# Performance work log

Hardware: AMD Instinct MI355X
Metric: run time of the kernel (lower is better)

Reference implementation:

```python
import jax, jax.numpy as jnp
import numpy as np

B, S, D, NH = 2, 1024, 2048, 8
QK, V, I = 1024, 2048, 8192  # qk_dim = D/2, v_dim = D, intermediate = 4D
CAP = 15.0
EPS = 1e-6


def setup_inputs() -> dict:
    key = jax.random.key(0)
    ks = jax.random.split(key, 12)
    sc = D ** -0.5
    return {
        "x": jax.random.normal(ks[0], (B, S, D), jnp.float32),
        "Wq": jax.random.normal(ks[1], (D, QK), jnp.float32) * sc,
        "Wk": jax.random.normal(ks[2], (D, QK), jnp.float32) * sc,
        "Wv": jax.random.normal(ks[3], (D, V), jnp.float32) * sc,
        "Wo": jax.random.normal(ks[4], (D, V), jnp.float32) * sc,
        "Wi": jax.random.normal(ks[5], (D, NH), jnp.float32) * sc,
        "bi": -10.0 * jnp.ones((NH,), jnp.float32),   # xLSTM input-gate bias init
        "Wf": jax.random.normal(ks[6], (D, NH), jnp.float32) * sc,
        "bf": jnp.linspace(3.0, 6.0, NH, dtype=jnp.float32),  # forget-gate bias init
        "mh_norm_w": jnp.ones((V,), jnp.float32),
        "Wout": jax.random.normal(ks[7], (V, D), jnp.float32) * (V ** -0.5),
        "rms1_w": jnp.ones((D,), jnp.float32),
        "Wgate": jax.random.normal(ks[8], (D, I), jnp.float32) * sc,
        "Wup": jax.random.normal(ks[9], (D, I), jnp.float32) * sc,
        "Wdown": jax.random.normal(ks[10], (I, D), jnp.float32) * (I ** -0.5),
        "rms2_w": jnp.ones((D,), jnp.float32),
    }


def soft_cap(x, cap=CAP):
    return cap * jnp.tanh(x / cap)


def rms_norm(x, w, eps=EPS):
    xf = x.astype(jnp.float32)
    var = jnp.mean(xf * xf, axis=-1, keepdims=True)
    return (w * (xf * jax.lax.rsqrt(var + eps))).astype(x.dtype)


def mlstm_stabilized(q, k, v, i, f):
    # q,k: [B,NH,S,DQK]; v: [B,NH,S,DV]; i,f: [B,NH,S] (soft-capped preacts)
    dqk = q.shape[-1]
    logf = jax.nn.log_sigmoid(f.astype(jnp.float32))
    lfc = jnp.cumsum(logf, axis=-1)                         # [B,NH,S]
    tri = jnp.tril(jnp.ones((S, S), bool))
    # log decay D[t,s] = sum_{j=s+1..t} log sig(f_j) + i_s  (causal)
    logD = jnp.where(tri, lfc[..., :, None] - lfc[..., None, :], -jnp.inf) + i[..., None, :]
    m = jnp.max(logD, axis=-1, keepdims=True)               # [B,NH,S,1] stabilizer
    Dm = jnp.exp(logD - m)
    scores = jnp.einsum("bhsd,bhtd->bhst", q, k) * (dqk ** -0.5) * Dm
    n = jnp.maximum(jnp.abs(scores.sum(-1, keepdims=True)), jnp.exp(-m))
    return jnp.einsum("bhst,bhtv->bhsv", scores, v) / (n + EPS)  # [B,NH,S,DV]


def xlstm_layer(x, Wq, Wk, Wv, Wo, Wi, bi, Wf, bf, mh_norm_w, Wout):
    q = (x @ Wq).reshape(B, S, NH, -1).transpose(0, 2, 1, 3)
    k = (x @ Wk).reshape(B, S, NH, -1).transpose(0, 2, 1, 3)
    v = (x @ Wv).reshape(B, S, NH, -1).transpose(0, 2, 1, 3)
    o_preact = x @ Wo                                       # [B,S,V]
    i = soft_cap(x @ Wi + bi).transpose(0, 2, 1)            # [B,NH,S]
    f = soft_cap(x @ Wf + bf).transpose(0, 2, 1)
    h = mlstm_stabilized(q, k, v, i, f)                     # [B,NH,S,DV]
    h = h.transpose(0, 2, 1, 3)                             # [B,S,NH,DV]
    # multi-head RMS norm over per-head value dim
    hf = h.astype(jnp.float32)
    var = jnp.mean(hf * hf, axis=-1, keepdims=True)
    hn = (hf * jax.lax.rsqrt(var + EPS)).reshape(B, S, V) * mh_norm_w
    h_out = jax.nn.sigmoid(o_preact) * hn                   # output gate
    return h_out @ Wout


def reference(x, Wq, Wk, Wv, Wo, Wi, bi, Wf, bf, mh_norm_w, Wout, rms1_w,
              Wgate, Wup, Wdown, rms2_w):
    residual = x
    h = xlstm_layer(x, Wq, Wk, Wv, Wo, Wi, bi, Wf, bf, mh_norm_w, Wout)
    h = residual + rms_norm(h, rms1_w)
    mlp = (jax.nn.silu(h @ Wgate) * (h @ Wup)) @ Wdown
    return h + rms_norm(mlp, rms2_w)
```

## Files before the change

kernel.cpp:

```cpp
#include <hip/hip_runtime.h>
#include <hip/hip_bf16.h>

#define TOKENS 2048
#define DMODEL 2048
#define SEQ    1024
#define QKVO   6144

typedef __attribute__((ext_vector_type(8))) short bf16x8;
typedef __attribute__((ext_vector_type(4))) short bf16x4;
typedef __attribute__((ext_vector_type(4))) float f32x4;
typedef __attribute__((ext_vector_type(8))) unsigned short u16x8;
typedef __attribute__((ext_vector_type(4))) unsigned short u16x4;

__device__ __forceinline__ float sigmoidf_(float x) { return 1.f / (1.f + expf(-x)); }
__device__ __forceinline__ float softcapf_(float x) { return 15.f * tanhf(x * (1.f / 15.f)); }
__device__ __forceinline__ float logsigf_(float x) {
  return (x >= 0.f) ? -log1pf(expf(-x)) : (x - log1pf(expf(x)));
}
__device__ __forceinline__ unsigned short f2bf(float f) {
  unsigned u = __builtin_bit_cast(unsigned, f);
  u += 0x7FFFu + ((u >> 16) & 1u);
  return (unsigned short)(u >> 16);
}
__device__ __forceinline__ float bf2f(unsigned short b) {
  unsigned u = ((unsigned)b) << 16;
  return __builtin_bit_cast(float, u);
}

typedef __attribute__((address_space(3))) void lds_void;
typedef const __attribute__((address_space(1))) void gmem_void;
__device__ __forceinline__ void gload16(const void* g, void* l) {
  __builtin_amdgcn_global_load_lds((gmem_void*)g, (lds_void*)l, 16, 0, 0);
}
__device__ __forceinline__ unsigned lds_off(const void* p) {
  return (unsigned)(size_t)(__attribute__((address_space(3))) const void*)p;
}

#if defined(__has_builtin)
#if __has_builtin(__builtin_amdgcn_mfma_f32_16x16x16bf16_1k)
#define HAVE_MFMA16 1
#endif
#endif

__device__ __forceinline__ f32x4 mfma16_bf16(bf16x4 a, bf16x4 b, f32x4 c) {
#ifdef HAVE_MFMA16
  return __builtin_amdgcn_mfma_f32_16x16x16bf16_1k(a, b, c, 0, 0, 0);
#else
  f32x4 d;
  asm volatile("v_mfma_f32_16x16x16_bf16 %0, %1, %2, %3"
               : "=v"(d) : "v"(a), "v"(b), "v"(c));
  return d;
#endif
}

__device__ __forceinline__ bf16x4 tr_read(unsigned addr) {
  bf16x4 d;
  asm volatile("ds_read_b64_tr_b16 %0, %1" : "=v"(d) : "v"(addr));
  return d;
}

__device__ __forceinline__ void remap_block(int& bm, int& bn) {
  const int nbx = gridDim.x, nby = gridDim.y;
  const int bid = blockIdx.y * nbx + blockIdx.x;
  const int q = (nbx * nby) >> 3;
  const int lid = (bid & 7) * q + (bid >> 3);
  bm = lid % nby;
  bn = lid / nby;
}

template <int EPI>
__global__ __launch_bounds__(512) void gemm256(
    const unsigned short* __restrict__ A, const unsigned short* __restrict__ BT,
    void* __restrict__ Cout, int M, int N, int K, int ldk) {
  __shared__ unsigned short lds[3][2][8192];
  const int tid = threadIdx.x;
  int bm, bn;
  remap_block(bm, bn);
  const int m0 = bm * 256, n0 = bn * 256;
  const int wid = tid >> 6, lane = tid & 63;
  const int wr = wid >> 2, wc = wid & 3;
  const int fr = lane & 15, fq = lane >> 4;
  const size_t kz = (size_t)blockIdx.z * K;

  const f32x4 zero = {0.f, 0.f, 0.f, 0.f};
  f32x4 acc[8][4];
#pragma unroll
  for (int m = 0; m < 8; ++m)
#pragma unroll
    for (int n = 0; n < 4; ++n) acc[m][n] = zero;

  const int sr = tid >> 2;
  const int sc = tid & 3;
  const int sgc = sc ^ ((sr + (sr >> 2)) & 3);
  const unsigned short* Asrc = A + kz + (size_t)(m0 + sr) * ldk + sgc * 8;
  const unsigned short* Bsrc = BT + kz + (size_t)(n0 + sr) * ldk + sgc * 8;
  const size_t hstep = (size_t)128 * ldk;
  const int ldst = sr * 32 + sc * 8;

  const int rsw = (fq ^ ((fr + (fr >> 2)) & 3)) * 8;
  const int arow0 = wr * 128 + fr;
  const int brow0 = wc * 64 + fr;

  auto stage = [&](int t) {
    const size_t ko = (size_t)t * 32;
    const int bs = t % 3;
    gload16(Asrc + ko, &lds[bs][0][ldst]);
    gload16(Asrc + ko + hstep, &lds[bs][0][4096 + ldst]);
    gload16(Bsrc + ko, &lds[bs][1][ldst]);
    gload16(Bsrc + ko + hstep, &lds[bs][1][4096 + ldst]);
  };

  const int NT = K >> 5;
  stage(0);
  stage(1);

  for (int t = 0; t < NT; ++t) {
    if (t + 1 < NT) {
      asm volatile("s_waitcnt vmcnt(4)" ::: "memory");
    } else {
      asm volatile("s_waitcnt vmcnt(0)" ::: "memory");
    }
    __builtin_amdgcn_s_barrier();
    if (t + 2 < NT) stage(t + 2);
    const int b = t % 3;
    const unsigned short* la = &lds[b][0][0];
    const unsigned short* lb = &lds[b][1][0];
    bf16x8 bfm[4], af[4];
#pragma unroll
    for (int n = 0; n < 4; ++n)
      bfm[n] = *(const bf16x8*)&lb[(brow0 + n * 16) * 32 + rsw];
#pragma unroll
    for (int m = 0; m < 4; ++m)
      af[m] = *(const bf16x8*)&la[(arow0 + m * 16) * 32 + rsw];
    __builtin_amdgcn_s_setprio(1);
#pragma unroll
    for (int m = 0; m < 4; ++m)
#pragma unroll
      for (int n = 0; n < 4; ++n)
        acc[m][n] = __builtin_amdgcn_mfma_f32_16x16x32_bf16(af[m], bfm[n],
                                                            acc[m][n], 0, 0, 0);
    __builtin_amdgcn_s_setprio(0);
#pragma unroll
    for (int m = 0; m < 4; ++m)
      af[m] = *(const bf16x8*)&la[(arow0 + 64 + m * 16) * 32 + rsw];
    __builtin_amdgcn_s_setprio(1);
#pragma unroll
    for (int m = 0; m < 4; ++m)
#pragma unroll
      for (int n = 0; n < 4; ++n)
        acc[4 + m][n] = __builtin_amdgcn_mfma_f32_16x16x32_bf16(
            af[m], bfm[n], acc[4 + m][n], 0, 0, 0);
    __builtin_amdgcn_s_setprio(0);
  }

  const int orow = m0 + wr * 128 + fq * 4;
  const int ocol = n0 + wc * 64 + fr;
#pragma unroll
  for (int m = 0; m < 8; ++m) {
#pragma unroll
    for (int n = 0; n < 4; ++n) {
      const int cc = ocol + n * 16;
#pragma unroll
      for (int j = 0; j < 4; ++j) {
        const int r = orow + m * 16 + j;
        float v = acc[m][n][j];
        if (EPI == 0) {
          ((float*)Cout + (size_t)blockIdx.z * M * N)[(size_t)r * N + cc] = v;
        } else {
          ((unsigned short*)Cout)[(size_t)r * N + cc] = f2bf(v);
        }
      }
    }
  }
}

__global__ __launch_bounds__(512) void gemm_dual(
    const unsigned short* __restrict__ A, const unsigned short* __restrict__ BT1,
    const unsigned short* __restrict__ BT2, unsigned short* __restrict__ Cout,
    int M, int N, int K) {
  __shared__ unsigned short lds[3][16384];
  const int tid = threadIdx.x;
  int bm, bn;
  remap_block(bm, bn);
  const int m0 = bm * 256, n0 = bn * 128;
  const int wid = tid >> 6, lane = tid & 63;
  const int wr = wid >> 2, wc = wid & 3;
  const int fr = lane & 15, fq = lane >> 4;

  const f32x4 zero = {0.f, 0.f, 0.f, 0.f};
  f32x4 acc1[8][2], acc2[8][2];
#pragma unroll
  for (int m = 0; m < 8; ++m)
#pragma unroll
    for (int n = 0; n < 2; ++n) { acc1[m][n] = zero; acc2[m][n] = zero; }

  const int sr = tid >> 2;
  const int sc = tid & 3;
  const int sgc = sc ^ ((sr + (sr >> 2)) & 3);
  const unsigned short* Asrc = A + (size_t)(m0 + sr) * K + sgc * 8;
  const unsigned short* B1src = BT1 + (size_t)(n0 + sr) * K + sgc * 8;
  const unsigned short* B2src = BT2 + (size_t)(n0 + sr) * K + sgc * 8;
  const size_t hstep = (size_t)128 * K;
  const int ldst = sr * 32 + sc * 8;

  const int rsw = (fq ^ ((fr + (fr >> 2)) & 3)) * 8;
  const int arow0 = wr * 128 + fr;
  const int brow0 = wc * 32 + fr;

  auto stage = [&](int t) {
    const size_t ko = (size_t)t * 32;
    const int bs = t % 3;
    gload16(Asrc + ko, &lds[bs][ldst]);
    gload16(Asrc + ko + hstep, &lds[bs][4096 + ldst]);
    gload16(B1src + ko, &lds[bs][8192 + ldst]);
    gload16(B2src + ko, &lds[bs][12288 + ldst]);
  };

  const int NT = K >> 5;
  stage(0);
  stage(1);

  for (int t = 0; t < NT; ++t) {
    if (t + 1 < NT) {
      asm volatile("s_waitcnt vmcnt(4)" ::: "memory");
    } else {
      asm volatile("s_waitcnt vmcnt(0)" ::: "memory");
    }
    __builtin_amdgcn_s_barrier();
    if (t + 2 < NT) stage(t + 2);
    const int b = t % 3;
    const unsigned short* la = &lds[b][0];
    bf16x8 b1[2], b2[2], af[4];
#pragma unroll
    for (int n = 0; n < 2; ++n) {
      b1[n] = *(const bf16x8*)&la[8192 + (brow0 + n * 16) * 32 + rsw];
      b2[n] = *(const bf16x8*)&la[12288 + (brow0 + n * 16) * 32 + rsw];
    }
#pragma unroll
    for (int m = 0; m < 4; ++m)
      af[m] = *(const bf16x8*)&la[(arow0 + m * 16) * 32 + rsw];
    __builtin_amdgcn_s_setprio(1);
#pragma unroll
    for (int m = 0; m < 4; ++m)
#pragma unroll
      for (int n = 0; n < 2; ++n) {
        acc1[m][n] = __builtin_amdgcn_mfma_f32_16x16x32_bf16(af[m], b1[n],
                                                             acc1[m][n], 0, 0, 0);
        acc2[m][n] = __builtin_amdgcn_mfma_f32_16x16x32_bf16(af[m], b2[n],
                                                             acc2[m][n], 0, 0, 0);
      }
    __builtin_amdgcn_s_setprio(0);
#pragma unroll
    for (int m = 0; m < 4; ++m)
      af[m] = *(const bf16x8*)&la[(arow0 + 64 + m * 16) * 32 + rsw];
    __builtin_amdgcn_s_setprio(1);
#pragma unroll
    for (int m = 0; m < 4; ++m)
#pragma unroll
      for (int n = 0; n < 2; ++n) {
        acc1[4 + m][n] = __builtin_amdgcn_mfma_f32_16x16x32_bf16(
            af[m], b1[n], acc1[4 + m][n], 0, 0, 0);
        acc2[4 + m][n] = __builtin_amdgcn_mfma_f32_16x16x32_bf16(
            af[m], b2[n], acc2[4 + m][n], 0, 0, 0);
      }
    __builtin_amdgcn_s_setprio(0);
  }

  const int orow = m0 + wr * 128 + fq * 4;
  const int ocol = n0 + wc * 32 + fr;
#pragma unroll
  for (int m = 0; m < 8; ++m) {
#pragma unroll
    for (int n = 0; n < 2; ++n) {
      const int cc = ocol + n * 16;
#pragma unroll
      for (int j = 0; j < 4; ++j) {
        const int r = orow + m * 16 + j;
        const float g = acc1[m][n][j];
        const float u = acc2[m][n][j];
        Cout[(size_t)r * N + cc] = f2bf(g * sigmoidf_(g) * u);
      }
    }
  }
}

template <int EPI>
__global__ __launch_bounds__(256) void gemm_bf16(
    const unsigned short* __restrict__ A, const unsigned short* __restrict__ BT,
    void* __restrict__ Cout, int M, int N, int K) {
  __shared__ unsigned short As[2][128 * 32];
  __shared__ unsigned short Bs[2][128 * 32];
  const int tid = threadIdx.x;
  int bm, bn;
  remap_block(bm, bn);
  const int m0 = bm * 128;
  const int n0 = bn * 128;
  const int wid = tid >> 6;
  const int lane = tid & 63;
  const int wr = wid >> 1, wc = wid & 1;
  const int fr = lane & 15, fq = lane >> 4;

  const f32x4 zero = {0.f, 0.f, 0.f, 0.f};
  f32x4 acc[4][4];
#pragma unroll
  for (int m = 0; m < 4; ++m)
#pragma unroll
    for (int n = 0; n < 4; ++n) acc[m][n] = zero;

  const int srow = tid >> 2;
  const int sc = tid & 3;
  const int sgc = sc ^ ((srow + (srow >> 2)) & 3);
  const int scol = sgc * 8;
  const unsigned short* Ag0 = A + (size_t)(m0 + srow) * K + scol;
  const unsigned short* Ag1 = A + (size_t)(m0 + 64 + srow) * K + scol;
  const unsigned short* Bg0 = BT + (size_t)(n0 + srow) * K + scol;
  const unsigned short* Bg1 = BT + (size_t)(n0 + 64 + srow) * K + scol;
  const int rsw = (fq ^ ((fr + (fr >> 2)) & 3)) * 8;

  gload16(Ag0, &As[0][tid * 8]);
  gload16(Ag1, &As[0][2048 + tid * 8]);
  gload16(Bg0, &Bs[0][tid * 8]);
  gload16(Bg1, &Bs[0][2048 + tid * 8]);
  __syncthreads();

  const int nt = K >> 5;
  for (int t = 0; t < nt; ++t) {
    const int cur = t & 1;
    if (t + 1 < nt) {
      const int k0 = (t + 1) << 5;
      gload16(Ag0 + k0, &As[cur ^ 1][tid * 8]);
      gload16(Ag1 + k0, &As[cur ^ 1][2048 + tid * 8]);
      gload16(Bg0 + k0, &Bs[cur ^ 1][tid * 8]);
      gload16(Bg1 + k0, &Bs[cur ^ 1][2048 + tid * 8]);
    }
    bf16x8 af[4], bfm[4];
#pragma unroll
    for (int m = 0; m < 4; ++m)
      af[m] = *(const bf16x8*)&As[cur][(wr * 64 + m * 16 + fr) * 32 + rsw];
#pragma unroll
    for (int n = 0; n < 4; ++n)
      bfm[n] = *(const bf16x8*)&Bs[cur][(wc * 64 + n * 16 + fr) * 32 + rsw];
    __builtin_amdgcn_s_setprio(1);
#pragma unroll
    for (int m = 0; m < 4; ++m)
#pragma unroll
      for (int n = 0; n < 4; ++n)
        acc[m][n] = __builtin_amdgcn_mfma_f32_16x16x32_bf16(af[m], bfm[n],
                                                            acc[m][n], 0, 0, 0);
    __builtin_amdgcn_s_setprio(0);
    __syncthreads();
  }

  const int orow = m0 + wr * 64 + fq * 4;
  const int ocol = n0 + wc * 64 + fr;
#pragma unroll
  for (int m = 0; m < 4; ++m) {
#pragma unroll
    for (int n = 0; n < 4; ++n) {
      const int cc = ocol + n * 16;
#pragma unroll
      for (int j = 0; j < 4; ++j) {
        const int r = orow + m * 16 + j;
        float v = acc[m][n][j];
        if (EPI == 0) ((float*)Cout)[(size_t)r * N + cc] = v;
        else ((unsigned short*)Cout)[(size_t)r * N + cc] = f2bf(v);
      }
    }
  }
}

__device__ __forceinline__ void castT_body(
    const float* __restrict__ W, unsigned short* __restrict__ WT, int K, int N) {
  __shared__ float tile[128][65];
  const int n0 = blockIdx.x * 64, k0 = blockIdx.y * 128;
  const int rr = threadIdx.x >> 4;
  const int c4 = (threadIdx.x & 15) * 4;
#pragma unroll
  for (int p = 0; p < 8; ++p) {
    const int r = p * 16 + rr;
    float4 v = *(const float4*)&W[(size_t)(k0 + r) * N + n0 + c4];
    tile[r][c4 + 0] = v.x; tile[r][c4 + 1] = v.y;
    tile[r][c4 + 2] = v.z; tile[r][c4 + 3] = v.w;
  }
  __syncthreads();
  const int kc = (threadIdx.x & 15) * 8;
#pragma unroll
  for (int p = 0; p < 4; ++p) {
    const int n = p * 16 + rr;
    u16x8 o;
#pragma unroll
    for (int j = 0; j < 8; ++j) o[j] = f2bf(tile[kc + j][n]);
    *(u16x8*)&WT[(size_t)(n0 + n) * K + k0 + kc] = o;
  }
}

__global__ __launch_bounds__(256) void castT_kernel(
    const float* __restrict__ W, unsigned short* __restrict__ WT, int K, int N) {
  castT_body(W, WT, K, N);
}

__global__ __launch_bounds__(256) void castT4_kernel(
    const float* __restrict__ Wq, const float* __restrict__ Wk,
    const float* __restrict__ Wv, const float* __restrict__ Wo,
    unsigned short* __restrict__ WT) {
  const int z = blockIdx.z;
  const float* src;
  unsigned short* dst;
  int N;
  if (z == 0)      { src = Wq; dst = WT;                          N = 1024; }
  else if (z == 1) { src = Wk; dst = WT + (size_t)1024 * 2048;    N = 1024; }
  else if (z == 2) { src = Wv; dst = WT + (size_t)2048 * 2048;    N = 2048; }
  else             { src = Wo; dst = WT + (size_t)4096 * 2048;    N = 2048; }
  if (blockIdx.x * 64 >= N) return;
  castT_body(src, dst, 2048, N);
}

__global__ __launch_bounds__(256) void castT2_kernel(
    const float* __restrict__ Wgate, const float* __restrict__ Wup,
    unsigned short* __restrict__ WT1, unsigned short* __restrict__ WT2) {
  if (blockIdx.z == 0) castT_body(Wgate, WT1, 2048, 8192);
  else castT_body(Wup, WT2, 2048, 8192);
}

__global__ __launch_bounds__(256) void gatesT_kernel(
    const float* __restrict__ Wi, const float* __restrict__ Wf,
    float* __restrict__ WT) {
  const int idx = blockIdx.x * 256 + threadIdx.x;
  const int row = idx >> 11;
  const int d = idx & 2047;
  const float* W = (row < 8) ? Wi : Wf;
  WT[idx] = W[d * 8 + (row & 7)];
}

__global__ __launch_bounds__(256) void gates_kernel(
    const float* __restrict__ x, const float* __restrict__ WT,
    const float* __restrict__ bi, const float* __restrict__ bf,
    float* __restrict__ icap, float* __restrict__ fls,
    unsigned short* __restrict__ xb) {
  const int t = blockIdx.x;
  const int tid = threadIdx.x;
  __shared__ float xs[2048];
  *(float4*)&xs[tid * 4] = *(const float4*)&x[(size_t)t * 2048 + tid * 4];
  *(float4*)&xs[1024 + tid * 4] =
      *(const float4*)&x[(size_t)t * 2048 + 1024 + tid * 4];
  __syncthreads();
  {
    u16x8 o;
#pragma unroll
    for (int j = 0; j < 8; ++j) o[j] = f2bf(xs[tid * 8 + j]);
    *(u16x8*)&xb[(size_t)t * 2048 + tid * 8] = o;
  }
  const int wave = tid >> 6, lane = tid & 63;
  const int b = t >> 10, s = t & 1023;
  for (int gg = wave; gg < 16; gg += 4) {
    const int head = gg & 7;
    const int isF = gg >> 3;
    const float* Wrow = WT + (size_t)gg * 2048;
    float acc = 0.f;
#pragma unroll
    for (int it = 0; it < 8; ++it) {
      const float4 w4 = *(const float4*)&Wrow[it * 256 + lane * 4];
      const float4 x4 = *(const float4*)&xs[it * 256 + lane * 4];
      acc = fmaf(x4.x, w4.x, acc);
      acc = fmaf(x4.y, w4.y, acc);
      acc = fmaf(x4.z, w4.z, acc);
      acc = fmaf(x4.w, w4.w, acc);
    }
#pragma unroll
    for (int m = 32; m > 0; m >>= 1) acc += __shfl_down(acc, m, 64);
    if (lane == 0) {
      const size_t o = (size_t)(b * 8 + head) * 1024 + s;
      if (isF) fls[o] = logsigf_(softcapf_(acc + bf[head]));
      else icap[o] = softcapf_(acc + bi[head]);
    }
  }
}

__global__ __launch_bounds__(1024) void scan_kernel(
    const float* __restrict__ icap, const float* __restrict__ fls,
    float* __restrict__ lfc, float* __restrict__ garr, float* __restrict__ mx) {
  const int bh = blockIdx.x;
  const int tid = threadIdx.x;
  __shared__ float sm[1024];
  sm[tid] = fls[(size_t)bh * 1024 + tid];
  __syncthreads();
  for (int off = 1; off < 1024; off <<= 1) {
    float v = sm[tid];
    if (tid >= off) v += sm[tid - off];
    __syncthreads();
    sm[tid] = v;
    __syncthreads();
  }
  const float l = sm[tid];
  lfc[(size_t)bh * 1024 + tid] = l;
  const float g = icap[(size_t)bh * 1024 + tid] - l;
  garr[(size_t)bh * 1024 + tid] = g;
  __syncthreads();
  sm[tid] = g;
  __syncthreads();
  for (int off = 1; off < 1024; off <<= 1) {
    float v = sm[tid];
    if (tid >= off) v = fmaxf(v, sm[tid - off]);
    __syncthreads();
    sm[tid] = v;
    __syncthreads();
  }
  mx[(size_t)bh * 1024 + tid] = sm[tid];
}

__global__ __launch_bounds__(128) void mlstm_mfma_kernel(
    const unsigned short* __restrict__ qkvob,
    const float* __restrict__ garr, const float* __restrict__ lfc,
    const float* __restrict__ mx, const float* __restrict__ mhw,
    unsigned short* __restrict__ houtb) {
  __shared__ unsigned short k_lds[32 * 128];
  __shared__ unsigned short v_lds[32 * 256];
  const int tid = threadIdx.x;
  const int lane = tid & 63;
  const int w = tid >> 6;
  const int bh = blockIdx.y;
  const int b = bh >> 3, hh = bh & 7;
  const int tb = (blockIdx.y < 8) ? blockIdx.x : (31 - blockIdx.x);
  const int fr = lane & 15, fq = lane >> 4;
  const int tw = tb * 32 + w * 16 + fr;
  const size_t tokT = (size_t)(b * SEQ + tw);
  const float scale = 0.08838834764831845f;

  bf16x8 qf[4];
#pragma unroll
  for (int kd = 0; kd < 4; ++kd)
    qf[kd] = *(const bf16x8*)&qkvob[tokT * QKVO + hh * 128 + kd * 32 + fq * 8];

  const float Mt = mx[(size_t)bh * SEQ + tw];
  const float mt = lfc[(size_t)bh * SEQ + tw] + Mt;

  f32x4 acc[16];
  const f32x4 zero = {0.f, 0.f, 0.f, 0.f};
#pragma unroll
  for (int D = 0; D < 16; ++D) acc[D] = zero;
  float asum = 0.f;

  const unsigned vbase = lds_off(v_lds);
  const int nsb = tb + 1;

  for (int sb = 0; sb < nsb; ++sb) {
    const int s0 = sb * 32;
    if (sb) __syncthreads();
#pragma unroll
    for (int it = 0; it < 4; ++it) {
      const int ck = it * 128 + tid;
      const int s = ck >> 4, c = ck & 15;
      const int cg = c ^ (s & 7);
      gload16(&qkvob[(size_t)(b * SEQ + s0 + s) * QKVO + 1024 + hh * 128 + cg * 8],
              &k_lds[ck * 8]);
    }
#pragma unroll
    for (int it = 0; it < 8; ++it) {
      const int cv = it * 128 + tid;
      const int W_ = cv >> 9, D = (cv >> 5) & 15, g = (cv >> 3) & 3,
                jj = (cv >> 1) & 3, c2 = cv & 1;
      const int s = W_ * 16 + g * 4 + jj;
      gload16(&qkvob[(size_t)(b * SEQ + s0 + s) * QKVO + 2048 + hh * 256 +
                     D * 16 + c2 * 8],
              &v_lds[cv * 8]);
    }
    __syncthreads();

#pragma unroll
    for (int st = 0; st < 2; ++st) {
      f32x4 cfrag = zero;
      const int srow = st * 16 + fr;
#pragma unroll
      for (int kd = 0; kd < 4; ++kd) {
        const int cc = (kd * 4 + fq) ^ (srow & 7);
        const bf16x8 kf = *(const bf16x8*)&k_lds[srow * 128 + cc * 8];
        cfrag = __builtin_amdgcn_mfma_f32_16x16x32_bf16(kf, qf[kd], cfrag, 0, 0, 0);
      }
      const int sbase = s0 + st * 16 + fq * 4;
      const float4 g4 = *(const float4*)&garr[(size_t)bh * SEQ + sbase];
      float wv[4];
      wv[0] = (sbase + 0 <= tw) ? cfrag[0] * scale * __expf(g4.x - Mt) : 0.f;
      wv[1] = (sbase + 1 <= tw) ? cfrag[1] * scale * __expf(g4.y - Mt) : 0.f;
      wv[2] = (sbase + 2 <= tw) ? cfrag[2] * scale * __expf(g4.z - Mt) : 0.f;
      wv[3] = (sbase + 3 <= tw) ? cfrag[3] * scale * __expf(g4.w - Mt) : 0.f;
      asum += wv[0] + wv[1] + wv[2] + wv[3];
      bf16x4 pf;
      pf[0] = (short)f2bf(wv[0]); pf[1] = (short)f2bf(wv[1]);
      pf[2] = (short)f2bf(wv[2]); pf[3] = (short)f2bf(wv[3]);

#pragma unroll
      for (int Dg = 0; Dg < 2; ++Dg) {
        bf16x4 vf[8];
#pragma unroll
        for (int D = 0; D < 8; ++D)
          vf[D] = tr_read(vbase + (st * 4096 + (Dg * 8 + D) * 256) * 2 + lane * 8);
        asm volatile("s_waitcnt lgkmcnt(0)" ::: "memory");
        __builtin_amdgcn_sched_barrier(0);
#pragma unroll
        for (int D = 0; D < 8; ++D)
          acc[Dg * 8 + D] = mfma16_bf16(vf[D], pf, acc[Dg * 8 + D]);
      }
    }
  }

  asum += __shfl_xor(asum, 16, 64);
  asum += __shfl_xor(asum, 32, 64);
  const float nrm = fmaxf(fabsf(asum), __expf(-mt));
  const float inv = 1.f / (nrm + 1e-6f);
  asm volatile("s_nop 7\n\ts_nop 7" ::);

  float hv[16][4];
  float ss = 0.f;
#pragma unroll
  for (int D = 0; D < 16; ++D)
#pragma unroll
    for (int j = 0; j < 4; ++j) {
      const float v = acc[D][j] * inv;
      hv[D][j] = v;
      ss += v * v;
    }
  ss += __shfl_xor(ss, 16, 64);
  ss += __shfl_xor(ss, 32, 64);
  const float rinv = rsqrtf(ss * (1.f / 256.f) + 1e-6f);
  unsigned short* hrow = &houtb[tokT * 2048 + hh * 256];
  const unsigned short* orow = &qkvob[tokT * QKVO + 4096 + hh * 256];
  const float* mrow = &mhw[hh * 256];
#pragma unroll
  for (int D = 0; D < 16; ++D) {
    const int d0 = D * 16 + fq * 4;
    const float4 m4 = *(const float4*)&mrow[d0];
    const u16x4 o4 = *(const u16x4*)&orow[d0];
    u16x4 res;
    res[0] = f2bf(hv[D][0] * rinv * m4.x * sigmoidf_(bf2f(o4[0])));
    res[1] = f2bf(hv[D][1] * rinv * m4.y * sigmoidf_(bf2f(o4[1])));
    res[2] = f2bf(hv[D][2] * rinv * m4.z * sigmoidf_(bf2f(o4[2])));
    res[3] = f2bf(hv[D][3] * rinv * m4.w * sigmoidf_(bf2f(o4[3])));
    *(u16x4*)&hrow[d0] = res;
  }
}

template <int EMIT_BF16, int NY>
__global__ __launch_bounds__(256) void addrms_kernel(
    const float* __restrict__ base_, const float* __restrict__ y0,
    const float* __restrict__ y1, const float* __restrict__ y2,
    const float* __restrict__ y3, const float* __restrict__ w,
    float* __restrict__ outp, unsigned short* __restrict__ outb) {
  const int t = blockIdx.x;
  const int tid = threadIdx.x;
  __shared__ float red[4];
  const size_t boff = (size_t)t * 2048 + tid * 8;
  float vals[8];
  *(float4*)&vals[0] = *(const float4*)&y0[boff];
  *(float4*)&vals[4] = *(const float4*)&y0[boff + 4];
  if (NY == 4) {
    float v1[8];
    *(float4*)&v1[0] = *(const float4*)&y1[boff];
    *(float4*)&v1[4] = *(const float4*)&y1[boff + 4];
#pragma unroll
    for (int j = 0; j < 8; ++j) vals[j] += v1[j];
    *(float4*)&v1[0] = *(const float4*)&y2[boff];
    *(float4*)&v1[4] = *(const float4*)&y2[boff + 4];
#pragma unroll
    for (int j = 0; j < 8; ++j) vals[j] += v1[j];
    *(float4*)&v1[0] = *(const float4*)&y3[boff];
    *(float4*)&v1[4] = *(const float4*)&y3[boff + 4];
#pragma unroll
    for (int j = 0; j < 8; ++j) vals[j] += v1[j];
  }
  float ss = 0.f;
#pragma unroll
  for (int j = 0; j < 8; ++j) ss += vals[j] * vals[j];
#pragma unroll
  for (int m = 32; m > 0; m >>= 1) ss += __shfl_xor(ss, m, 64);
  if ((tid & 63) == 0) red[tid >> 6] = ss;
  __syncthreads();
  ss = red[0] + red[1] + red[2] + red[3];
  const float rinv = rsqrtf(ss * (1.f / 2048.f) + 1e-6f);
  float bv[8];
  *(float4*)&bv[0] = *(const float4*)&base_[boff];
  *(float4*)&bv[4] = *(const float4*)&base_[boff + 4];
  float res[8];
  u16x8 rb;
#pragma unroll
  for (int j = 0; j < 8; ++j) {
    res[j] = bv[j] + vals[j] * rinv * w[tid * 8 + j];
    if (EMIT_BF16) rb[j] = f2bf(res[j]);
  }
  *(float4*)&outp[boff] = *(float4*)&res[0];
  *(float4*)&outp[boff + 4] = *(float4*)&res[4];
  if (EMIT_BF16) *(u16x8*)&outb[boff] = rb;
}

extern "C" void kernel_launch(void* const* d_in, const int* in_sizes, int n_in,
                              void* d_out, int out_size, void* d_ws,
                              size_t ws_size, hipStream_t stream) {
  const float* x = (const float*)d_in[0];
  const float* Wq = (const float*)d_in[1];
  const float* Wk = (const float*)d_in[2];
  const float* Wv = (const float*)d_in[3];
  const float* Wo = (const float*)d_in[4];
  const float* Wi = (const float*)d_in[5];
  const float* bi = (const float*)d_in[6];
  const float* Wf = (const float*)d_in[7];
  const float* bf = (const float*)d_in[8];
  const float* mhw = (const float*)d_in[9];
  const float* Wout = (const float*)d_in[10];
  const float* rms1 = (const float*)d_in[11];
  const float* Wgate = (const float*)d_in[12];
  const float* Wup = (const float*)d_in[13];
  const float* Wdown = (const float*)d_in[14];
  const float* rms2 = (const float*)d_in[15];
  float* out = (float*)d_out;
  char* base = (char*)d_ws;
  const size_t MBy = 1024 * 1024;

  unsigned short* W = (unsigned short*)(base);
  unsigned short* actb = (unsigned short*)(base + 32 * MBy);
  float* gs = (float*)(base + 48 * MBy);
  unsigned short* houtb = (unsigned short*)(base + 56 * MBy);
  float* f1 = (float*)(base + 64 * MBy);
  unsigned short* WupT = (unsigned short*)(base + 80 * MBy);
  float* mlp = (float*)(base + 80 * MBy);
  unsigned short* xb = (unsigned short*)(base + 112 * MBy);
  unsigned short* f1b = (unsigned short*)(base + 112 * MBy);
  unsigned short* qkvob = (unsigned short*)(base + 120 * MBy);
  float* attn = (float*)(base + 120 * MBy);
  float* icap = gs;
  float* fls = gs + 16384;
  float* lfc = gs + 32768;
  float* garr = gs + 49152;
  float* mxp = gs + 65536;
  float* gwT = gs + 81920;

  const dim3 blk(256);

  gatesT_kernel<<<128, blk, 0, stream>>>(Wi, Wf, gwT);
  gates_kernel<<<TOKENS, blk, 0, stream>>>(x, gwT, bi, bf, icap, fls, xb);
  scan_kernel<<<16, 1024, 0, stream>>>(icap, fls, lfc, garr, mxp);

  castT4_kernel<<<dim3(32, 16, 4), blk, 0, stream>>>(Wq, Wk, Wv, Wo, W);
  gemm256<1><<<dim3(24, 8), dim3(512), 0, stream>>>(
      xb, W, qkvob, TOKENS, 6144, 2048, 2048);

  mlstm_mfma_kernel<<<dim3(32, 16), dim3(128), 0, stream>>>(
      qkvob, garr, lfc, mxp, mhw, houtb);

  castT_kernel<<<dim3(32, 16), blk, 0, stream>>>(Wout, W, 2048, 2048);
  gemm_bf16<0><<<dim3(16, 16), blk, 0, stream>>>(houtb, W, attn, TOKENS, 2048,
                                                 2048);

  addrms_kernel<1, 1><<<TOKENS, blk, 0, stream>>>(
      x, attn, nullptr, nullptr, nullptr, rms1, f1, f1b);

  castT2_kernel<<<dim3(128, 16, 2), blk, 0, stream>>>(Wgate, Wup, W, WupT);
  gemm_dual<<<dim3(64, 8), dim3(512), 0, stream>>>(f1b, W, WupT, actb,
                                                   TOKENS, 8192, 2048);

  castT_kernel<<<dim3(32, 64), blk, 0, stream>>>(Wdown, W, 8192, 2048);
  gemm256<0><<<dim3(8, 8, 4), dim3(512), 0, stream>>>(
      actb, W, mlp, TOKENS, 2048, 2048, 8192);

  addrms_kernel<0, 4><<<TOKENS, blk, 0, stream>>>(
      f1, mlp, mlp + 4194304, mlp + 8388608, mlp + 12582912, rms2, out,
      nullptr);
}
```

Before: 497.1 us.

## Use 256x128 tiles with split-K 2 for down projection, merge Wout cast

```diff
diff --git a/kernel.cpp b/kernel.cpp
--- a/kernel.cpp
+++ b/kernel.cpp
@@ -68,26 +68,28 @@
   bn = lid / nby;
 }
 
-template <int EPI>
+template <int EPI, int NBF>
 __global__ __launch_bounds__(512) void gemm256(
     const unsigned short* __restrict__ A, const unsigned short* __restrict__ BT,
     void* __restrict__ Cout, int M, int N, int K, int ldk) {
-  __shared__ unsigned short lds[3][2][8192];
+  constexpr int BN = 64 * NBF;
+  constexpr int BSZ = BN * 32;
+  __shared__ unsigned short lds[3][8192 + BSZ];
   const int tid = threadIdx.x;
   int bm, bn;
   remap_block(bm, bn);
-  const int m0 = bm * 256, n0 = bn * 256;
+  const int m0 = bm * 256, n0 = bn * BN;
   const int wid = tid >> 6, lane = tid & 63;
   const int wr = wid >> 2, wc = wid & 3;
   const int fr = lane & 15, fq = lane >> 4;
   const size_t kz = (size_t)blockIdx.z * K;
 
   const f32x4 zero = {0.f, 0.f, 0.f, 0.f};
-  f32x4 acc[8][4];
+  f32x4 acc[8][NBF];
 #pragma unroll
   for (int m = 0; m < 8; ++m)
 #pragma unroll
-    for (int n = 0; n < 4; ++n) acc[m][n] = zero;
+    for (int n = 0; n < NBF; ++n) acc[m][n] = zero;
 
   const int sr = tid >> 2;
   const int sc = tid & 3;
@@ -99,15 +101,15 @@
 
   const int rsw = (fq ^ ((fr + (fr >> 2)) & 3)) * 8;
   const int arow0 = wr * 128 + fr;
-  const int brow0 = wc * 64 + fr;
+  const int brow0 = wc * (16 * NBF) + fr;
 
   auto stage = [&](int t) {
     const size_t ko = (size_t)t * 32;
     const int bs = t % 3;
-    gload16(Asrc + ko, &lds[bs][0][ldst]);
-    gload16(Asrc + ko + hstep, &lds[bs][0][4096 + ldst]);
-    gload16(Bsrc + ko, &lds[bs][1][ldst]);
-    gload16(Bsrc + ko + hstep, &lds[bs][1][4096 + ldst]);
+    gload16(Asrc + ko, &lds[bs][ldst]);
+    gload16(Asrc + ko + hstep, &lds[bs][4096 + ldst]);
+    gload16(Bsrc + ko, &lds[bs][8192 + ldst]);
+    if (NBF == 4) gload16(Bsrc + ko + hstep, &lds[bs][8192 + 4096 + ldst]);
   };
 
   const int NT = K >> 5;
@@ -116,18 +118,22 @@
 
   for (int t = 0; t < NT; ++t) {
     if (t + 1 < NT) {
-      asm volatile("s_waitcnt vmcnt(4)" ::: "memory");
+      if (NBF == 4) {
+        asm volatile("s_waitcnt vmcnt(4)" ::: "memory");
+      } else {
+        asm volatile("s_waitcnt vmcnt(3)" ::: "memory");
+      }
     } else {
       asm volatile("s_waitcnt vmcnt(0)" ::: "memory");
     }
     __builtin_amdgcn_s_barrier();
     if (t + 2 < NT) stage(t + 2);
     const int b = t % 3;
-    const unsigned short* la = &lds[b][0][0];
-    const unsigned short* lb = &lds[b][1][0];
-    bf16x8 bfm[4], af[4];
-#pragma unroll
-    for (int n = 0; n < 4; ++n)
+    const unsigned short* la = &lds[b][0];
+    const unsigned short* lb = &lds[b][8192];
+    bf16x8 bfm[NBF], af[4];
+#pragma unroll
+    for (int n = 0; n < NBF; ++n)
       bfm[n] = *(const bf16x8*)&lb[(brow0 + n * 16) * 32 + rsw];
 #pragma unroll
     for (int m = 0; m < 4; ++m)
@@ -136,7 +142,7 @@
 #pragma unroll
     for (int m = 0; m < 4; ++m)
 #pragma unroll
-      for (int n = 0; n < 4; ++n)
+      for (int n = 0; n < NBF; ++n)
         acc[m][n] = __builtin_amdgcn_mfma_f32_16x16x32_bf16(af[m], bfm[n],
                                                             acc[m][n], 0, 0, 0);
     __builtin_amdgcn_s_setprio(0);
@@ -147,18 +153,18 @@
 #pragma unroll
     for (int m = 0; m < 4; ++m)
 #pragma unroll
-      for (int n = 0; n < 4; ++n)
+      for (int n = 0; n < NBF; ++n)
         acc[4 + m][n] = __builtin_amdgcn_mfma_f32_16x16x32_bf16(
             af[m], bfm[n], acc[4 + m][n], 0, 0, 0);
     __builtin_amdgcn_s_setprio(0);
   }
 
   const int orow = m0 + wr * 128 + fq * 4;
-  const int ocol = n0 + wc * 64 + fr;
+  const int ocol = n0 + wc * (16 * NBF) + fr;
 #pragma unroll
   for (int m = 0; m < 8; ++m) {
 #pragma unroll
-    for (int n = 0; n < 4; ++n) {
+    for (int n = 0; n < NBF; ++n) {
       const int cc = ocol + n * 16;
 #pragma unroll
       for (int j = 0; j < 4; ++j) {
@@ -399,18 +405,19 @@
   castT_body(W, WT, K, N);
 }
 
-__global__ __launch_bounds__(256) void castT4_kernel(
+__global__ __launch_bounds__(256) void castT5_kernel(
     const float* __restrict__ Wq, const float* __restrict__ Wk,
     const float* __restrict__ Wv, const float* __restrict__ Wo,
-    unsigned short* __restrict__ WT) {
+    const float* __restrict__ Wout, unsigned short* __restrict__ WT) {
   const int z = blockIdx.z;
   const float* src;
   unsigned short* dst;
   int N;
-  if (z == 0)      { src = Wq; dst = WT;                          N = 1024; }
-  else if (z == 1) { src = Wk; dst = WT + (size_t)1024 * 2048;    N = 1024; }
-  else if (z == 2) { src = Wv; dst = WT + (size_t)2048 * 2048;    N = 2048; }
-  else             { src = Wo; dst = WT + (size_t)4096 * 2048;    N = 2048; }
+  if (z == 0)      { src = Wq;   dst = WT;                        N = 1024; }
+  else if (z == 1) { src = Wk;   dst = WT + (size_t)1024 * 2048;  N = 1024; }
+  else if (z == 2) { src = Wv;   dst = WT + (size_t)2048 * 2048;  N = 2048; }
+  else if (z == 3) { src = Wo;   dst = WT + (size_t)4096 * 2048;  N = 2048; }
+  else             { src = Wout; dst = WT + (size_t)6144 * 2048;  N = 2048; }
   if (blockIdx.x * 64 >= N) return;
   castT_body(src, dst, 2048, N);
 }
@@ -642,8 +649,7 @@
 template <int EMIT_BF16, int NY>
 __global__ __launch_bounds__(256) void addrms_kernel(
     const float* __restrict__ base_, const float* __restrict__ y0,
-    const float* __restrict__ y1, const float* __restrict__ y2,
-    const float* __restrict__ y3, const float* __restrict__ w,
+    const float* __restrict__ y1, const float* __restrict__ w,
     float* __restrict__ outp, unsigned short* __restrict__ outb) {
   const int t = blockIdx.x;
   const int tid = threadIdx.x;
@@ -652,18 +658,10 @@
   float vals[8];
   *(float4*)&vals[0] = *(const float4*)&y0[boff];
   *(float4*)&vals[4] = *(const float4*)&y0[boff + 4];
-  if (NY == 4) {
+  if (NY == 2) {
     float v1[8];
     *(float4*)&v1[0] = *(const float4*)&y1[boff];
     *(float4*)&v1[4] = *(const float4*)&y1[boff + 4];
-#pragma unroll
-    for (int j = 0; j < 8; ++j) vals[j] += v1[j];
-    *(float4*)&v1[0] = *(const float4*)&y2[boff];
-    *(float4*)&v1[4] = *(const float4*)&y2[boff + 4];
-#pragma unroll
-    for (int j = 0; j < 8; ++j) vals[j] += v1[j];
-    *(float4*)&v1[0] = *(const float4*)&y3[boff];
-    *(float4*)&v1[4] = *(const float4*)&y3[boff + 4];
 #pragma unroll
     for (int j = 0; j < 8; ++j) vals[j] += v1[j];
   }
@@ -738,29 +736,28 @@
   gates_kernel<<<TOKENS, blk, 0, stream>>>(x, gwT, bi, bf, icap, fls, xb);
   scan_kernel<<<16, 1024, 0, stream>>>(icap, fls, lfc, garr, mxp);
 
-  castT4_kernel<<<dim3(32, 16, 4), blk, 0, stream>>>(Wq, Wk, Wv, Wo, W);
-  gemm256<1><<<dim3(24, 8), dim3(512), 0, stream>>>(
+  castT5_kernel<<<dim3(32, 16, 5), blk, 0, stream>>>(Wq, Wk, Wv, Wo, Wout, W);
+
+  gemm256<1, 4><<<dim3(24, 8), dim3(512), 0, stream>>>(
       xb, W, qkvob, TOKENS, 6144, 2048, 2048);
 
   mlstm_mfma_kernel<<<dim3(32, 16), dim3(128), 0, stream>>>(
       qkvob, garr, lfc, mxp, mhw, houtb);
 
-  castT_kernel<<<dim3(32, 16), blk, 0, stream>>>(Wout, W, 2048, 2048);
-  gemm_bf16<0><<<dim3(16, 16), blk, 0, stream>>>(houtb, W, attn, TOKENS, 2048,
-                                                 2048);
-
-  addrms_kernel<1, 1><<<TOKENS, blk, 0, stream>>>(
-      x, attn, nullptr, nullptr, nullptr, rms1, f1, f1b);
+  gemm_bf16<0><<<dim3(16, 16), blk, 0, stream>>>(
+      houtb, W + (size_t)6144 * 2048, attn, TOKENS, 2048, 2048);
+
+  addrms_kernel<1, 1><<<TOKENS, blk, 0, stream>>>(x, attn, nullptr, rms1, f1,
+                                                  f1b);
 
   castT2_kernel<<<dim3(128, 16, 2), blk, 0, stream>>>(Wgate, Wup, W, WupT);
   gemm_dual<<<dim3(64, 8), dim3(512), 0, stream>>>(f1b, W, WupT, actb,
                                                    TOKENS, 8192, 2048);
 
   castT_kernel<<<dim3(32, 64), blk, 0, stream>>>(Wdown, W, 8192, 2048);
-  gemm256<0><<<dim3(8, 8, 4), dim3(512), 0, stream>>>(
-      actb, W, mlp, TOKENS, 2048, 2048, 8192);
-
-  addrms_kernel<0, 4><<<TOKENS, blk, 0, stream>>>(
-      f1, mlp, mlp + 4194304, mlp + 8388608, mlp + 12582912, rms2, out,
-      nullptr);
-}
+  gemm256<0, 2><<<dim3(16, 8, 2), dim3(512), 0, stream>>>(
+      actb, W, mlp, TOKENS, 2048, 4096, 8192);
+
+  addrms_kernel<0, 2><<<TOKENS, blk, 0, stream>>>(f1, mlp, mlp + 4194304, rms2,
+                                                  out, nullptr);
+}
```

Result: no change. 499.6 us (+0.5%).
